# Kernel tuning notes

Measured on AMD Instinct MI355X. Metric: run time of the kernel, lower is better.

## Reference

```python
import jax, jax.numpy as jnp
import numpy as np

N_NODES = 20000
N_EDGES = 320000
N_RELS = 200
DESC_LEN = 16
DIM_G = 64
DIM_WORD = 300
DIM_HIDDEN = 256
H_DIR = DIM_HIDDEN // 2  # per-direction GRU hidden
N_CLASS = 2000
V_WORD = 30000
V_DESC = 30000
B, T = 4, 32


def setup_inputs() -> dict:
    key = jax.random.key(0)
    ks = jax.random.split(key, 24)
    inp = {}
    # index tensors (pad token is 0; generate tokens in [1, V) so all positions valid)
    inp['questions'] = jax.random.randint(ks[0], (B, T), 1, V_WORD)
    inp['node_descs'] = jax.random.randint(ks[1], (N_NODES, DESC_LEN), 1, V_DESC)
    inp['edge_src'] = jax.random.randint(ks[2], (N_EDGES,), 0, N_NODES)
    inp['edge_dst'] = jax.random.randint(ks[3], (N_EDGES,), 0, N_NODES)
    inp['edge_type'] = jax.random.randint(ks[4], (N_EDGES,), 0, N_RELS)
    # embeddings (normal with std 1/sqrt(dim) as in original init)
    inp['emb_word'] = jax.random.normal(ks[5], (V_WORD, DIM_WORD)) / np.sqrt(DIM_WORD)
    inp['emb_desc'] = jax.random.normal(ks[6], (V_DESC, DIM_G)) / np.sqrt(DIM_G)
    # BiGRU params (gates order r,z,n; concatenated along last dim)
    s = 0.1
    inp['Wx_f'] = jax.random.normal(ks[7], (DIM_WORD, 3 * H_DIR)) * s
    inp['Wh_f'] = jax.random.normal(ks[8], (H_DIR, 3 * H_DIR)) * s
    inp['bx_f'] = jnp.zeros((3 * H_DIR,))
    inp['bh_f'] = jnp.zeros((3 * H_DIR,))
    inp['Wx_b'] = jax.random.normal(ks[9], (DIM_WORD, 3 * H_DIR)) * s
    inp['Wh_b'] = jax.random.normal(ks[10], (H_DIR, 3 * H_DIR)) * s
    inp['bx_b'] = jnp.zeros((3 * H_DIR,))
    inp['bh_b'] = jnp.zeros((3 * H_DIR,))
    # lin_h_to_g (kaiming-ish scale)
    inp['W_hg'] = jax.random.normal(ks[11], (DIM_HIDDEN, DIM_G)) * np.sqrt(2.0 / DIM_HIDDEN)
    inp['b_hg'] = jnp.zeros((DIM_G,))
    # RGCN basis decomposition
    inp['bases'] = jax.random.normal(ks[12], (1, DIM_G, DIM_G)) * np.sqrt(1.0 / DIM_G)
    inp['w_comp'] = jax.random.normal(ks[13], (N_RELS, 1))
    inp['rgcn_bias'] = jnp.zeros((DIM_G,))
    # classifier
    inp['W1'] = jax.random.normal(ks[14], (DIM_G + DIM_HIDDEN, 1024)) * np.sqrt(2.0 / (DIM_G + DIM_HIDDEN))
    inp['b1'] = jnp.zeros((1024,))
    inp['W2'] = jax.random.normal(ks[15], (1024, N_CLASS)) * np.sqrt(2.0 / 1024)
    inp['b2'] = jnp.zeros((N_CLASS,))
    return inp


def _gru_last_hidden(x, mask, Wx, Wh, bx, bh):
    """Run a GRU over time; hidden only updates where mask is True.
    x: [B,T,D], mask: [B,T]. Returns final hidden [B,H]."""
    bsz = x.shape[0]
    h0 = jnp.zeros((bsz, Wh.shape[0]), x.dtype)
    gx_all = x @ Wx + bx  # [B,T,3H] precompute input gates

    def step(h, inputs):
        gx, mt = inputs  # [B,3H], [B]
        gh = h @ Wh + bh
        xr, xz, xn = jnp.split(gx, 3, axis=-1)
        hr, hz, hn = jnp.split(gh, 3, axis=-1)
        r = jax.nn.sigmoid(xr + hr)
        z = jax.nn.sigmoid(xz + hz)
        n = jnp.tanh(xn + r * hn)
        h_new = (1.0 - z) * n + z * h
        h = jnp.where(mt[:, None], h_new, h)
        return h, None

    hT, _ = jax.lax.scan(step, h0, (gx_all.transpose(1, 0, 2), mask.T))
    return hT


def _rel_graph_conv(h, edge_src, edge_dst, edge_type, bases, w_comp, bias):
    """Basis-decomposed RGCN layer (DGL RelGraphConv, norm=None, no self-loop).
    h: [B,N,G]. W_r = sum_k w_comp[r,k] * bases[k]."""
    n = h.shape[1]
    # project through each basis first: [B,N,K,O]
    hb = jnp.einsum('bng,kgo->bnko', h, bases)
    # per-edge message: gather src, combine with relation coefficients -> [B,E,O]
    msg = jnp.einsum('beko,ek->beo', hb[:, edge_src], w_comp[edge_type])
    # scatter-add to destination nodes
    agg = jax.vmap(lambda m: jax.ops.segment_sum(m, edge_dst, num_segments=n))(msg)
    return jax.nn.relu(agg + bias)


def reference(questions, node_descs, edge_src, edge_dst, edge_type,
              emb_word, emb_desc,
              Wx_f, Wh_f, bx_f, bh_f, Wx_b, Wh_b, bx_b, bh_b,
              W_hg, b_hg, bases, w_comp, rgcn_bias,
              W1, b1, W2, b2):
    # ---- question encoding (BiGRU over non-pad tokens; pad id = 0) ----
    mask = questions != 0  # [B,T]
    x = emb_word[questions]  # [B,T,Dw] (dropout is identity at eval)
    hf = _gru_last_hidden(x, mask, Wx_f, Wh_f, bx_f, bh_f)
    hb = _gru_last_hidden(x[:, ::-1], mask[:, ::-1], Wx_b, Wh_b, bx_b, bh_b)
    q_emb = jnp.concatenate([hf, hb], axis=-1)  # [B, dim_hidden]

    # ---- attention-weighted node features from descriptions ----
    desc_emb = emb_desc[node_descs]          # [N,L,G]
    q_g = q_emb @ W_hg + b_hg                # [B,G]
    attn1 = jax.nn.softmax(jnp.einsum('nlg,bg->bnl', desc_emb, q_g), axis=-1)
    node_feat = jnp.einsum('bnl,nlg->bng', attn1, desc_emb)  # [B,N,G]

    # ---- one RGCN hidden layer over the KB graph ----
    node_feat = _rel_graph_conv(node_feat, edge_src, edge_dst, edge_type,
                                bases, w_comp, rgcn_bias)

    # ---- attention pooling over nodes ----
    attn2 = jax.nn.softmax(jnp.einsum('bng,bg->bn', node_feat, q_g), axis=1)
    node_agg = jnp.einsum('bn,bng->bg', attn2, node_feat)    # [B,G]

    # ---- classifier ----
    feat = jnp.concatenate([node_agg, q_emb], axis=-1)       # [B, G+H]
    logits = jax.nn.relu(feat @ W1 + b1) @ W2 + b2           # [B, n_class]
    return logits
```

## Files before the change

### kernel.cpp

```cpp
#include <hip/hip_runtime.h>
#include <hip/hip_bf16.h>
#include <math.h>

typedef __hip_bfloat16 bf16;

#define NNODES 20000
#define NEDGES 320000
#define DLEN   16
#define G      64
#define DW     300
#define DH     256
#define HD     128
#define G3     384
#define NCLS   2000
#define NB     4
#define TT     32
#define VDESC  30000
#define A2BLK  1024
#define A2MID  64

#define NBLK_CVT   384
#define NBLK_GX2   1536
#define NBLK_DESCB (VDESC / 16)
#define NBLK_HIST  ((NEDGES + 255) / 256)
#define NBLK_SCAT  ((NEDGES + 255) / 256)
#define NBLK_DQ    ((VDESC + 63) / 64)

__device__ __forceinline__ float ld(const float* p, size_t i) { return p[i]; }
__device__ __forceinline__ float ld(const bf16* p, size_t i) { return __bfloat162float(p[i]); }
__device__ __forceinline__ void st(float* p, size_t i, float v) { p[i] = v; }
__device__ __forceinline__ void st(bf16* p, size_t i, float v) { p[i] = __float2bfloat16(v); }
__device__ __forceinline__ float relu(float x) { return (x < 0.f) ? 0.f : x; }

struct __align__(8) bf4 { bf16 x, y, z, w; };

#define OFF_FLAG  ((size_t)0)
#define OFF_GX    (OFF_FLAG + 4)
#define OFF_WHF   (OFF_GX   + 2*NB*TT*G3)
#define OFF_QEMB  (OFF_WHF  + 2*HD*G3)
#define OFF_QG    (OFF_QEMB + NB*DH)
#define OFF_NF    (OFF_QG   + NB*G)
#define OFF_HB    (OFF_NF   + (size_t)NB*NNODES*G)
#define OFF_DESCB (OFF_HB   + (size_t)NB*NNODES*G)
#define OFF_DQ    (OFF_DESCB + (size_t)VDESC*G/2)
#define OFF_PART  (OFF_DQ   + (size_t)VDESC*NB)
#define OFF_PART2 (OFF_PART + (size_t)A2BLK*NB*66)
#define OFF_DEG   (OFF_PART2+ (size_t)A2MID*NB*66)
#define OFF_OFFS  (OFF_DEG  + NNODES)
#define OFF_RANK  (OFF_OFFS + NNODES + 8)
#define OFF_EPACK (OFF_RANK + NEDGES)
#define OFF_HID   (OFF_EPACK + 2*(size_t)NEDGES)

__global__ void k_init(const unsigned* probe, int* flag, int* deg) {
    int i = blockIdx.x * 256 + threadIdx.x;
    if (i < NNODES) deg[i] = 0;
    if (blockIdx.x == 0 && threadIdx.x < 64) {
        int cnt = 0;
        for (int k = threadIdx.x; k < 4096; k += 64) {
            unsigned lo = probe[k] & 0xFFFFu;
            unsigned e = (lo >> 7) & 0xFFu;
            cnt += (e >= 0x66u && e <= 0x7Eu) ? 1 : 0;
        }
#pragma unroll
        for (int off = 1; off < 64; off <<= 1) cnt += __shfl_xor(cnt, off, 64);
        if (threadIdx.x == 0) *flag = (2 * cnt > 4096) ? 1 : 0;
    }
}

template <typename T>
__device__ void cvt_body(int id, const void* Whf_, const void* Whb_, float* whf) {
    if (id >= 2 * HD * G3) return;
    int d = id / (HD * G3), r = id % (HD * G3);
    const T* W = (const T*)(d ? Whb_ : Whf_);
    whf[id] = ld(W, (size_t)r);
}

template <typename T>
__device__ void gx2_body(int bx2, const int* questions, const void* emb_word_,
                         const void* Wxf_, const void* bxf_,
                         const void* Wxb_, const void* bxb_, float* gx,
                         float* xs, float* psum) {
    int tid = threadIdx.x;
    int jt = bx2 % 6;
    int rid = bx2 / 6;
    int step = rid & 31;
    int b = (rid >> 5) & 3;
    int d = rid >> 7;
    int t = d ? (TT - 1 - step) : step;
    int tok = questions[b * TT + t];
    const T* row = (const T*)emb_word_ + (size_t)tok * DW;
    for (int k = tid; k < DW; k += 256) xs[k] = ld(row, (size_t)k);
    __syncthreads();
    int lane = tid & 63, phase = tid >> 6;
    int j = jt * 64 + lane;
    const T* Wx = (const T*)(d ? Wxb_ : Wxf_);
    float acc = 0.f;
    int k0 = phase * 75;
#pragma unroll 15
    for (int kk = 0; kk < 75; kk++) {
        int k = k0 + kk;
        acc += xs[k] * ld(Wx, (size_t)k * G3 + j);
    }
    psum[tid] = acc;
    __syncthreads();
    if (phase == 0) {
        const T* bx = (const T*)(d ? bxb_ : bxf_);
        float tot = ld(bx, (size_t)j)
                  + psum[lane] + psum[64 + lane] + psum[128 + lane] + psum[192 + lane];
        gx[(size_t)rid * G3 + j] = tot;
    }
}

template <typename T>
__device__ void descb_body(int bx3, const void* emb_desc_, const void* bases_,
                           bf16* descB, float* bsm, float* rsm) {
    int tid = threadIdx.x;
    const T* bases = (const T*)bases_;
    const T* desc = (const T*)emb_desc_;
    for (int i = tid; i < G * G; i += 256) bsm[(i >> 6) * 68 + (i & 63)] = ld(bases, (size_t)i);
    int r0 = bx3 * 16;
    for (int i = tid; i < 16 * G; i += 256) {
        int r = i >> 6, k = i & 63;
        rsm[r * 68 + k] = ld(desc, (size_t)(r0 + r) * G + k);
    }
    __syncthreads();
    int g = tid & 63, slot = tid >> 6;
#pragma unroll
    for (int it = 0; it < 4; it++) {
        int r = slot * 4 + it;
        float acc = 0.f;
#pragma unroll 8
        for (int k = 0; k < G; k++) acc = fmaf(rsm[r * 68 + k], bsm[k * 68 + g], acc);
        descB[(size_t)(r0 + r) * G + g] = __float2bfloat16(acc);
    }
}

__global__ void k_prep(const int* flag, const void* Whf, const void* Whb, float* whf,
                       const int* questions, const void* emb_word,
                       const void* Wxf, const void* bxf,
                       const void* Wxb, const void* bxb, float* gx,
                       const void* emb_desc, const void* bases, bf16* descB,
                       const int* edge_dst, int* deg, int* rank) {
    __shared__ __align__(16) float smem[64 * 68 + 16 * 68];
    int bx = blockIdx.x;
    int tid = threadIdx.x;
    if (bx < NBLK_CVT) {
        int id = bx * 256 + tid;
        if (*flag) cvt_body<bf16>(id, Whf, Whb, whf);
        else       cvt_body<float>(id, Whf, Whb, whf);
    } else if (bx < NBLK_CVT + NBLK_GX2) {
        int bx2 = bx - NBLK_CVT;
        float* xs = smem;
        float* psum = smem + 320;
        if (*flag) gx2_body<bf16>(bx2, questions, emb_word, Wxf, bxf, Wxb, bxb, gx, xs, psum);
        else       gx2_body<float>(bx2, questions, emb_word, Wxf, bxf, Wxb, bxb, gx, xs, psum);
    } else if (bx < NBLK_CVT + NBLK_GX2 + NBLK_DESCB) {
        int bx3 = bx - NBLK_CVT - NBLK_GX2;
        float* bsm = smem;
        float* rsm = smem + 64 * 68;
        if (*flag) descb_body<bf16>(bx3, emb_desc, bases, descB, bsm, rsm);
        else       descb_body<float>(bx3, emb_desc, bases, descB, bsm, rsm);
    } else {
        int e = (bx - NBLK_CVT - NBLK_GX2 - NBLK_DESCB) * 256 + tid;
        if (e < NEDGES) rank[e] = atomicAdd(&deg[edge_dst[e]], 1);
    }
}

template <typename T>
__device__ void gru_body(const int* questions, const float* gx, const float* whf,
                         const void* bhf_, const void* bhb_, float* qemb,
                         float* hsm, float* ghs) {
    int tid = threadIdx.x;
    int d = blockIdx.x >> 2, b = blockIdx.x & 3;
    int half = tid / G3, j = tid - half * G3;
    const float* wh = whf + (size_t)d * HD * G3 + (size_t)half * 64 * G3 + j;
    float w[64];
#pragma unroll
    for (int m = 0; m < 64; m++) w[m] = wh[(size_t)m * G3];
    const T* bh = (const T*)(d ? bhb_ : bhf_);
    float bhj = (half == 0) ? ld(bh, (size_t)j) : 0.f;
    if (tid < HD) hsm[tid] = 0.f;
    const float* gxb = gx + ((size_t)(d * NB + b)) * TT * G3;
    __syncthreads();
    const float4* h4 = (const float4*)(hsm + half * 64);
    for (int step = 0; step < TT; step++) {
        float acc = bhj;
#pragma unroll
        for (int m4 = 0; m4 < 16; m4++) {
            float4 hp = h4[m4];
            acc = fmaf(hp.x, w[4 * m4 + 0], acc);
            acc = fmaf(hp.y, w[4 * m4 + 1], acc);
            acc = fmaf(hp.z, w[4 * m4 + 2], acc);
            acc = fmaf(hp.w, w[4 * m4 + 3], acc);
        }
        ghs[half * G3 + j] = acc;
        __syncthreads();
        if (tid < HD) {
            const float* gxp = gxb + step * G3;
            int t = d ? (TT - 1 - step) : step;
            bool msk = questions[b * TT + t] != 0;
            float gr = ghs[tid] + ghs[G3 + tid];
            float gz = ghs[HD + tid] + ghs[G3 + HD + tid];
            float gn = ghs[2 * HD + tid] + ghs[G3 + 2 * HD + tid];
            float r = 1.f / (1.f + expf(-(gxp[tid] + gr)));
            float z = 1.f / (1.f + expf(-(gxp[HD + tid] + gz)));
            float n = tanhf(gxp[2 * HD + tid] + r * gn);
            float hn = (1.f - z) * n + z * hsm[tid];
            if (msk) hsm[tid] = hn;
        }
        __syncthreads();
    }
    if (tid < HD) qemb[b * DH + d * HD + tid] = hsm[tid];
}

__device__ void scan_body(const int* deg, int* offs, int* wtot) {
    int t = threadIdx.x;
    int lane = t & 63, wave = t >> 6;
    int c[27];
    int base = t * 27;
    int run = 0;
#pragma unroll
    for (int i = 0; i < 27; i++) {
        int v = (base + i < NNODES) ? deg[base + i] : 0;
        c[i] = run;
        run += v;
    }
    int myrun = run, inc = run;
#pragma unroll
    for (int off = 1; off < 64; off <<= 1) {
        int u = __shfl_up(inc, off, 64);
        if (lane >= off) inc += u;
    }
    if (lane == 63) wtot[wave] = inc;
    __syncthreads();
    if (t == 0) {
        int s = 0;
#pragma unroll
        for (int i = 0; i < 12; i++) { int v = wtot[i]; wtot[i] = s; s += v; }
        offs[NNODES] = s;
    }
    __syncthreads();
    int ebase = wtot[wave] + inc - myrun;
#pragma unroll
    for (int i = 0; i < 27; i++) {
        if (base + i < NNODES) offs[base + i] = ebase + c[i];
    }
}

__global__ __launch_bounds__(2 * G3) void k_gru(const int* flag, const int* questions,
                                                const float* gx, const float* whf,
                                                const void* bhf, const void* bhb, float* qemb,
                                                const int* deg, int* offs) {
    __shared__ __align__(16) float hsm[HD];
    __shared__ float ghs[2 * G3];
    __shared__ int wtot[12];
    if (blockIdx.x < 8) {
        if (*flag) gru_body<bf16>(questions, gx, whf, bhf, bhb, qemb, hsm, ghs);
        else       gru_body<float>(questions, gx, whf, bhf, bhb, qemb, hsm, ghs);
    } else {
        scan_body(deg, offs, wtot);
    }
}

template <typename T>
__device__ void qg_compute(const float* qemb, const void* W_hg_, const void* b_hg_,
                           float* out ) {
    int tid = threadIdx.x;
    int b = tid >> 6, g = tid & 63;
    const T* W = (const T*)W_hg_;
    float acc = ld((const T*)b_hg_, (size_t)g);
#pragma unroll 4
    for (int i = 0; i < DH; i++) acc += qemb[b * DH + i] * ld(W, (size_t)i * G + g);
    out[b * G + g] = acc;
}

template <typename T>
__device__ void dq_body(int chunk, const void* emb_desc_, const float* qgs, float* dq) {
    int tid = threadIdx.x;
    int ii = tid >> 2, b = tid & 3;
    int idx = chunk * 64 + ii;
    if (idx >= VDESC) return;
    const T* row = (const T*)emb_desc_ + (size_t)idx * G;
    const float* q = qgs + b * G;
    float acc = 0.f;
#pragma unroll 8
    for (int k = 0; k < G; k++) acc = fmaf(ld(row, (size_t)k), q[k], acc);
    dq[(size_t)idx * NB + b] = acc;
}

__global__ __launch_bounds__(256) void k_qg_dq(const int* flag, const float* qemb,
                                               const void* W_hg, const void* b_hg, float* qg,
                                               const void* emb_desc, float* dq) {
    __shared__ float qgs[NB * G];
    if (blockIdx.x == 0) {
        if (*flag) qg_compute<bf16>(qemb, W_hg, b_hg, qg);
        else       qg_compute<float>(qemb, W_hg, b_hg, qg);
        return;
    }
    if (*flag) qg_compute<bf16>(qemb, W_hg, b_hg, qgs);
    else       qg_compute<float>(qemb, W_hg, b_hg, qgs);
    __syncthreads();
    int chunk = blockIdx.x - 1;
    if (*flag) dq_body<bf16>(chunk, emb_desc, qgs, dq);
    else       dq_body<float>(chunk, emb_desc, qgs, dq);
}

template <typename T>
__device__ void scatter_body(int e, const int* src, const int* dst, const int* typ,
                             const void* w_comp_, const int* offs, const int* rank,
                             int2* epack) {
    if (e < NEDGES) {
        int pos = offs[dst[e]] + rank[e];
        int2 v;
        v.x = src[e];
        v.y = __float_as_int(ld((const T*)w_comp_, (size_t)typ[e]));
        epack[pos] = v;
    }
}

__device__ void attn1_body(int nb4, const int* node_descs, const float* dq,
                           const bf16* descB, bf16* hb16, float* attn_s, int* idxs) {
    int tid = threadIdx.x;
    int w = tid >> 6, lane = tid & 63;
    int n = nb4 * 4 + w;
    int b = lane >> 4, l = lane & 15;
    const int* nd = node_descs + n * DLEN;
    int idx = nd[l];
    float logit = dq[(size_t)idx * NB + b];
    float mx = logit;
#pragma unroll
    for (int off = 1; off < 16; off <<= 1) mx = fmaxf(mx, __shfl_xor(mx, off, 64));
    float e = expf(logit - mx);
    float s = e;
#pragma unroll
    for (int off = 1; off < 16; off <<= 1) s += __shfl_xor(s, off, 64);
    attn_s[w * 64 + lane] = e / s;
    if (lane < 16) idxs[w * 16 + lane] = idx;
    __syncthreads();
    float o0 = 0.f, o1 = 0.f, o2 = 0.f, o3 = 0.f;
#pragma unroll
    for (int ll = 0; ll < DLEN; ll++) {
        int row = idxs[w * 16 + ll];
        float v = __bfloat162float(descB[(size_t)row * G + lane]);
        o0 = fmaf(attn_s[w * 64 + ll], v, o0);
        o1 = fmaf(attn_s[w * 64 + 16 + ll], v, o1);
        o2 = fmaf(attn_s[w * 64 + 32 + ll], v, o2);
        o3 = fmaf(attn_s[w * 64 + 48 + ll], v, o3);
    }
    size_t baseo = (size_t)n * (NB * G) + lane;
    hb16[baseo + 0 * G] = __float2bfloat16(o0);
    hb16[baseo + 1 * G] = __float2bfloat16(o1);
    hb16[baseo + 2 * G] = __float2bfloat16(o2);
    hb16[baseo + 3 * G] = __float2bfloat16(o3);
}

__global__ __launch_bounds__(256) void k_sc_attn1(const int* flag,
                                                  const int* src, const int* dst, const int* typ,
                                                  const void* w_comp, const int* offs,
                                                  const int* rank, int2* epack,
                                                  const int* node_descs, const float* dq,
                                                  const bf16* descB, bf16* hb16) {
    __shared__ float attn_s[4 * 64];
    __shared__ int idxs[4 * DLEN];
    int bx = blockIdx.x;
    if (bx < NBLK_SCAT) {
        int e = bx * 256 + threadIdx.x;
        if (*flag) scatter_body<bf16>(e, src, dst, typ, w_comp, offs, rank, epack);
        else       scatter_body<float>(e, src, dst, typ, w_comp, offs, rank, epack);
    } else {
        attn1_body(bx - NBLK_SCAT, node_descs, dq, descB, hb16, attn_s, idxs);
    }
}

template <typename T>
__device__ void agg_body(const bf16* hb16, const int* offs, const int2* epack,
                         const void* bias_, bf16* out_nf16) {
    int tid = threadIdx.x;
    int b = tid >> 6, g = tid & 63;
    int dn = blockIdx.x;
    int s0 = offs[dn], s1 = offs[dn + 1];
    int boff = b * G + g;
    float acc = 0.f;
    int p = s0;
    for (; p + 15 < s1; p += 16) {
        int2 ev[16]; float x[16];
#pragma unroll
        for (int k = 0; k < 16; k++) ev[k] = epack[p + k];
#pragma unroll
        for (int k = 0; k < 16; k++)
            x[k] = __bfloat162float(hb16[(size_t)ev[k].x * (NB * G) + boff]);
#pragma unroll
        for (int k = 0; k < 16; k++) acc += __int_as_float(ev[k].y) * x[k];
    }
    for (; p + 7 < s1; p += 8) {
        int2 ev[8]; float x[8];
#pragma unroll
        for (int k = 0; k < 8; k++) ev[k] = epack[p + k];
#pragma unroll
        for (int k = 0; k < 8; k++)
            x[k] = __bfloat162float(hb16[(size_t)ev[k].x * (NB * G) + boff]);
#pragma unroll
        for (int k = 0; k < 8; k++) acc += __int_as_float(ev[k].y) * x[k];
    }
    for (; p + 3 < s1; p += 4) {
        int2 ev[4]; float x[4];
#pragma unroll
        for (int k = 0; k < 4; k++) ev[k] = epack[p + k];
#pragma unroll
        for (int k = 0; k < 4; k++)
            x[k] = __bfloat162float(hb16[(size_t)ev[k].x * (NB * G) + boff]);
#pragma unroll
        for (int k = 0; k < 4; k++) acc += __int_as_float(ev[k].y) * x[k];
    }
    for (; p < s1; p++) {
        int2 ev = epack[p];
        acc += __int_as_float(ev.y) * __bfloat162float(hb16[(size_t)ev.x * (NB * G) + boff]);
    }
    out_nf16[((size_t)b * NNODES + dn) * G + g] =
        __float2bfloat16(relu(acc + ld((const T*)bias_, (size_t)g)));
}
__global__ __launch_bounds__(256) void k_agg(const int* flag, const bf16* hb16, const int* offs,
                                             const int2* epack, const void* bias,
                                             bf16* out_nf16) {
    if (*flag) agg_body<bf16>(hb16, offs, epack, bias, out_nf16);
    else       agg_body<float>(hb16, offs, epack, bias, out_nf16);
}

__device__ __forceinline__ void a2_update(float& M, float& L, float& A, float p, float v) {
    if (p > M) {
        float s = expf(M - p);
        A *= s; L *= s; M = p;
    }
    float e = expf(p - M);
    L += e;
    A = fmaf(e, v, A);
}

__global__ __launch_bounds__(256) void k_attn2(const bf16* rg, const float* qg, float* part) {
    int tid = threadIdx.x;
    int b = tid >> 6, lane = tid & 63;
    float q = qg[b * G + lane];
    int chunk = (NNODES + A2BLK - 1) / A2BLK;
    int n0 = blockIdx.x * chunk;
    int n1 = min(n0 + chunk, NNODES);
    const bf16* base = rg + (size_t)b * NNODES * G + lane;
    float M = -3.4e38f, L = 0.f, A = 0.f;
    int n = n0;
    for (; n + 3 < n1; n += 4) {
        float v0 = __bfloat162float(base[(size_t)(n + 0) * G]);
        float v1 = __bfloat162float(base[(size_t)(n + 1) * G]);
        float v2 = __bfloat162float(base[(size_t)(n + 2) * G]);
        float v3 = __bfloat162float(base[(size_t)(n + 3) * G]);
        float p0 = v0 * q, p1 = v1 * q, p2 = v2 * q, p3 = v3 * q;
#pragma unroll
        for (int off = 32; off >= 1; off >>= 1) {
            p0 += __shfl_xor(p0, off, 64);
            p1 += __shfl_xor(p1, off, 64);
            p2 += __shfl_xor(p2, off, 64);
            p3 += __shfl_xor(p3, off, 64);
        }
        a2_update(M, L, A, p0, v0);
        a2_update(M, L, A, p1, v1);
        a2_update(M, L, A, p2, v2);
        a2_update(M, L, A, p3, v3);
    }
    for (; n < n1; n++) {
        float v = __bfloat162float(base[(size_t)n * G]);
        float p = v * q;
#pragma unroll
        for (int off = 32; off >= 1; off >>= 1) p += __shfl_xor(p, off, 64);
        a2_update(M, L, A, p, v);
    }
    float* pp = part + ((size_t)blockIdx.x * NB + b) * 66;
    if (lane == 0) { pp[0] = M; pp[1] = L; }
    pp[2 + lane] = A;
}

__global__ void k_attn2m(const float* part, float* part2) {
    int tid = threadIdx.x;
    int b = tid >> 6, lane = tid & 63;
    int grp = blockIdx.x;
    float M = -3.4e38f, L = 0.f, A = 0.f;
    for (int i = 0; i < A2BLK / A2MID; i++) {
        const float* pp = part + ((size_t)(grp * (A2BLK / A2MID) + i) * NB + b) * 66;
        float m = pp[0], l = pp[1], a = pp[2 + lane];
        float mn = fmaxf(M, m);
        float e1 = expf(M - mn), e2 = expf(m - mn);
        A = A * e1 + a * e2;
        L = L * e1 + l * e2;
        M = mn;
    }
    float* pq = part2 + ((size_t)grp * NB + b) * 66;
    if (lane == 0) { pq[0] = M; pq[1] = L; }
    pq[2 + lane] = A;
}

template <typename T>
__device__ void fc1_body(const float* part2, const float* qemb,
                         const void* W1_, const void* b1_, float* hid,
                         float* feat, float* psum) {
    int tid = threadIdx.x;
    int b = blockIdx.x >> 4, tile = blockIdx.x & 15;
    if (tid < 64) {
        float M = -3.4e38f, L = 0.f, A = 0.f;
        for (int p = 0; p < A2MID; p++) {
            const float* pp = part2 + ((size_t)p * NB + b) * 66;
            float m = pp[0], l = pp[1], a = pp[2 + tid];
            float mn = fmaxf(M, m);
            float e1 = expf(M - mn), e2 = expf(m - mn);
            A = A * e1 + a * e2;
            L = L * e1 + l * e2;
            M = mn;
        }
        feat[tid] = A / L;
        feat[tid + 256] = qemb[b * DH + tid + 192];
    } else {
        feat[tid] = qemb[b * DH + tid - G];
    }
    __syncthreads();
    int lane = tid & 63, phase = tid >> 6;
    int u = tile * 64 + lane;
    const T* W1 = (const T*)W1_;
    float acc = 0.f;
#pragma unroll 8
    for (int kk = 0; kk < 80; kk++) {
        int k = phase * 80 + kk;
        acc += feat[k] * ld(W1, (size_t)k * 1024 + u);
    }
    psum[tid] = acc;
    __syncthreads();
    if (phase == 0) {
        float tot = psum[lane] + psum[64 + lane] + psum[128 + lane] + psum[192 + lane]
                  + ld((const T*)b1_, (size_t)u);
        hid[b * 1024 + u] = relu(tot);
    }
}
__global__ __launch_bounds__(256) void k_fc1(const int* flag, const float* part2,
                                             const float* qemb, const void* W1, const void* b1,
                                             float* hid) {
    __shared__ float feat[320];
    __shared__ float psum[256];
    if (*flag) fc1_body<bf16>(part2, qemb, W1, b1, hid, feat, psum);
    else       fc1_body<float>(part2, qemb, W1, b1, hid, feat, psum);
}

template <typename T>
__device__ void fc2_body(const float* hid, const void* W2_, const void* b2_, void* out_,
                         float* hs, float* psum) {
    int tid = threadIdx.x;
    int tile = blockIdx.x;
#pragma unroll
    for (int i = 0; i < 16; i++) hs[tid + 256 * i] = hid[tid + 256 * i];
    __syncthreads();
    int lane = tid & 63, phase = tid >> 6;
    int c = tile * 64 + lane;
    bool ok = (c < NCLS);
    const T* W2 = (const T*)W2_;
    float a0 = 0.f, a1 = 0.f, a2 = 0.f, a3 = 0.f;
    if (ok) {
#pragma unroll 8
        for (int uu = 0; uu < 256; uu++) {
            int u = phase * 256 + uu;
            float w = ld(W2, (size_t)u * NCLS + c);
            a0 += hs[u] * w;
            a1 += hs[1024 + u] * w;
            a2 += hs[2048 + u] * w;
            a3 += hs[3072 + u] * w;
        }
    }
    psum[tid] = a0;
    psum[256 + tid] = a1;
    psum[512 + tid] = a2;
    psum[768 + tid] = a3;
    __syncthreads();
    if (phase == 0 && ok) {
        float bb = ld((const T*)b2_, (size_t)c);
#pragma unroll
        for (int b = 0; b < NB; b++) {
            float* ps = psum + b * 256;
            float tot = ps[lane] + ps[64 + lane] + ps[128 + lane] + ps[192 + lane] + bb;
            st((T*)out_, (size_t)b * NCLS + c, tot);
        }
    }
}
__global__ __launch_bounds__(256) void k_fc2(const int* flag, const float* hid,
                                             const void* W2, const void* b2v, void* out) {
    __shared__ float hs[4096];
    __shared__ float psum[1024];
    if (*flag) fc2_body<bf16>(hid, W2, b2v, out, hs, psum);
    else       fc2_body<float>(hid, W2, b2v, out, hs, psum);
}

extern "C" void kernel_launch(void* const* d_in, const int* in_sizes, int n_in,
                              void* d_out, int out_size, void* d_ws, size_t ws_size,
                              hipStream_t stream) {
    const int* questions  = (const int*)d_in[0];
    const int* node_descs = (const int*)d_in[1];
    const int* edge_src   = (const int*)d_in[2];
    const int* edge_dst   = (const int*)d_in[3];
    const int* edge_type  = (const int*)d_in[4];
    const void* emb_word  = d_in[5];
    const void* emb_desc  = d_in[6];
    const void* Wx_f = d_in[7];
    const void* Wh_f = d_in[8];
    const void* bx_f = d_in[9];
    const void* bh_f = d_in[10];
    const void* Wx_b = d_in[11];
    const void* Wh_b = d_in[12];
    const void* bx_b = d_in[13];
    const void* bh_b = d_in[14];
    const void* W_hg = d_in[15];
    const void* b_hg = d_in[16];
    const void* bases = d_in[17];
    const void* w_comp = d_in[18];
    const void* rgcn_bias = d_in[19];
    const void* W1 = d_in[20];
    const void* b1 = d_in[21];
    const void* W2 = d_in[22];
    const void* b2 = d_in[23];

    float* ws = (float*)d_ws;
    int*      flag  = (int*)(ws + OFF_FLAG);
    float*    gx    = ws + OFF_GX;
    float*    whf   = ws + OFF_WHF;
    float*    qemb  = ws + OFF_QEMB;
    float*    qg    = ws + OFF_QG;
    bf16*     nf16  = (bf16*)(ws + OFF_NF);
    bf16*     hb16  = (bf16*)(ws + OFF_HB);
    bf16*     descB = (bf16*)(ws + OFF_DESCB);
    float*    dq    = ws + OFF_DQ;
    float*    part  = ws + OFF_PART;
    float*    part2 = ws + OFF_PART2;
    int*      deg   = (int*)(ws + OFF_DEG);
    int*      offs  = (int*)(ws + OFF_OFFS);
    int*      rank  = (int*)(ws + OFF_RANK);
    int2*     epack = (int2*)(ws + OFF_EPACK);
    float*    hid   = ws + OFF_HID;

    hipLaunchKernelGGL(k_init, dim3(80), dim3(256), 0, stream,
                       (const unsigned*)emb_word, flag, deg);
    hipLaunchKernelGGL(k_prep,
                       dim3(NBLK_CVT + NBLK_GX2 + NBLK_DESCB + NBLK_HIST), dim3(256), 0, stream,
                       flag, Wh_f, Wh_b, whf,
                       questions, emb_word, Wx_f, bx_f, Wx_b, bx_b, gx,
                       emb_desc, bases, descB,
                       edge_dst, deg, rank);
    hipLaunchKernelGGL(k_gru, dim3(9), dim3(2 * G3), 0, stream,
                       flag, questions, gx, whf, bh_f, bh_b, qemb, deg, offs);
    hipLaunchKernelGGL(k_qg_dq, dim3(1 + NBLK_DQ), dim3(256), 0, stream,
                       flag, qemb, W_hg, b_hg, qg, emb_desc, dq);
    hipLaunchKernelGGL(k_sc_attn1, dim3(NBLK_SCAT + NNODES / 4), dim3(256), 0, stream,
                       flag, edge_src, edge_dst, edge_type, w_comp, offs, rank, epack,
                       node_descs, dq, descB, hb16);
    hipLaunchKernelGGL(k_agg, dim3(NNODES), dim3(256), 0, stream,
                       flag, hb16, offs, epack, rgcn_bias, nf16);
    hipLaunchKernelGGL(k_attn2, dim3(A2BLK), dim3(256), 0, stream, nf16, qg, part);
    hipLaunchKernelGGL(k_attn2m, dim3(A2MID), dim3(256), 0, stream, part, part2);
    hipLaunchKernelGGL(k_fc1, dim3(NB * 16), dim3(256), 0, stream,
                       flag, part2, qemb, W1, b1, hid);
    hipLaunchKernelGGL(k_fc2, dim3(32), dim3(256), 0, stream,
                       flag, hid, W2, b2, d_out);
}
```

Measured before the change: 305.4 us.

## Fuse RGCN aggregation with attention pooling, transpose W2 for wider fc2

Folds the attention-pooling online softmax into the RGCN aggregation kernel, so the bf16 node-feature tensor is never written and then read back. Each aggregation block now handles four destination nodes and emits one partial, and the merge kernel takes the larger partial count. The attn1 blocks each process four node groups. W2 is transposed into the workspace during the prep kernel so fc2 can run on 250 blocks with coalesced row reads and wave reductions, at the cost of an extra 8 MB transpose pass on every call.

```diff
diff --git a/kernel.cpp b/kernel.cpp
--- a/kernel.cpp
+++ b/kernel.cpp
@@ -16,14 +16,16 @@
 #define NB     4
 #define TT     32
 #define VDESC  30000
-#define A2BLK  1024
+#define NPART  5000
 #define A2MID  64
 
 #define NBLK_CVT   384
 #define NBLK_GX2   1536
 #define NBLK_DESCB (VDESC / 16)
 #define NBLK_HIST  ((NEDGES + 255) / 256)
+#define NBLK_W2T   (32 * 16)
 #define NBLK_SCAT  ((NEDGES + 255) / 256)
+#define NBLK_A1    (NNODES / 16)
 #define NBLK_DQ    ((VDESC + 63) / 64)
 
 __device__ __forceinline__ float ld(const float* p, size_t i) { return p[i]; }
@@ -32,24 +34,22 @@
 __device__ __forceinline__ void st(bf16* p, size_t i, float v) { p[i] = __float2bfloat16(v); }
 __device__ __forceinline__ float relu(float x) { return (x < 0.f) ? 0.f : x; }
 
-struct __align__(8) bf4 { bf16 x, y, z, w; };
-
 #define OFF_FLAG  ((size_t)0)
 #define OFF_GX    (OFF_FLAG + 4)
 #define OFF_WHF   (OFF_GX   + 2*NB*TT*G3)
 #define OFF_QEMB  (OFF_WHF  + 2*HD*G3)
 #define OFF_QG    (OFF_QEMB + NB*DH)
-#define OFF_NF    (OFF_QG   + NB*G)
-#define OFF_HB    (OFF_NF   + (size_t)NB*NNODES*G)
-#define OFF_DESCB (OFF_HB   + (size_t)NB*NNODES*G)
+#define OFF_HB    (OFF_QG   + NB*G)
+#define OFF_DESCB (OFF_HB   + (size_t)NB*NNODES*G/2)
 #define OFF_DQ    (OFF_DESCB + (size_t)VDESC*G/2)
 #define OFF_PART  (OFF_DQ   + (size_t)VDESC*NB)
-#define OFF_PART2 (OFF_PART + (size_t)A2BLK*NB*66)
+#define OFF_PART2 (OFF_PART + (size_t)NPART*NB*66)
 #define OFF_DEG   (OFF_PART2+ (size_t)A2MID*NB*66)
 #define OFF_OFFS  (OFF_DEG  + NNODES)
 #define OFF_RANK  (OFF_OFFS + NNODES + 8)
 #define OFF_EPACK (OFF_RANK + NEDGES)
 #define OFF_HID   (OFF_EPACK + 2*(size_t)NEDGES)
+#define OFF_W2T   (OFF_HID  + 4096)
 
 __global__ void k_init(const unsigned* probe, int* flag, int* deg) {
     int i = blockIdx.x * 256 + threadIdx.x;
@@ -135,12 +135,36 @@
     }
 }
 
+template <typename T>
+__device__ void w2t_body(int bx5, const void* W2_, float* w2t, float* tile ) {
+    int tid = threadIdx.x;
+    int ct = bx5 >> 4, ut = bx5 & 15;
+    int c0 = ct * 64, u0 = ut * 64;
+    int lane = tid & 63, slot = tid >> 6;
+    const T* W2 = (const T*)W2_;
+    int c = c0 + lane;
+    bool okc = (c < NCLS);
+#pragma unroll
+    for (int i = 0; i < 16; i++) {
+        int u = slot * 16 + i;
+        tile[u * 65 + lane] = okc ? ld(W2, (size_t)(u0 + u) * NCLS + c) : 0.f;
+    }
+    __syncthreads();
+#pragma unroll
+    for (int i = 0; i < 16; i++) {
+        int cl = slot * 16 + i;
+        if (c0 + cl < NCLS)
+            w2t[(size_t)(c0 + cl) * 1024 + u0 + lane] = tile[lane * 65 + cl];
+    }
+}
+
 __global__ void k_prep(const int* flag, const void* Whf, const void* Whb, float* whf,
                        const int* questions, const void* emb_word,
                        const void* Wxf, const void* bxf,
                        const void* Wxb, const void* bxb, float* gx,
                        const void* emb_desc, const void* bases, bf16* descB,
-                       const int* edge_dst, int* deg, int* rank) {
+                       const int* edge_dst, int* deg, int* rank,
+                       const void* W2, float* w2t) {
     __shared__ __align__(16) float smem[64 * 68 + 16 * 68];
     int bx = blockIdx.x;
     int tid = threadIdx.x;
@@ -160,9 +184,13 @@
         float* rsm = smem + 64 * 68;
         if (*flag) descb_body<bf16>(bx3, emb_desc, bases, descB, bsm, rsm);
         else       descb_body<float>(bx3, emb_desc, bases, descB, bsm, rsm);
-    } else {
+    } else if (bx < NBLK_CVT + NBLK_GX2 + NBLK_DESCB + NBLK_HIST) {
         int e = (bx - NBLK_CVT - NBLK_GX2 - NBLK_DESCB) * 256 + tid;
         if (e < NEDGES) rank[e] = atomicAdd(&deg[edge_dst[e]], 1);
+    } else {
+        int bx5 = bx - NBLK_CVT - NBLK_GX2 - NBLK_DESCB - NBLK_HIST;
+        if (*flag) w2t_body<bf16>(bx5, W2, w2t, smem);
+        else       w2t_body<float>(bx5, W2, w2t, smem);
     }
 }
 
@@ -368,62 +396,12 @@
         if (*flag) scatter_body<bf16>(e, src, dst, typ, w_comp, offs, rank, epack);
         else       scatter_body<float>(e, src, dst, typ, w_comp, offs, rank, epack);
     } else {
-        attn1_body(bx - NBLK_SCAT, node_descs, dq, descB, hb16, attn_s, idxs);
-    }
-}
-
-template <typename T>
-__device__ void agg_body(const bf16* hb16, const int* offs, const int2* epack,
-                         const void* bias_, bf16* out_nf16) {
-    int tid = threadIdx.x;
-    int b = tid >> 6, g = tid & 63;
-    int dn = blockIdx.x;
-    int s0 = offs[dn], s1 = offs[dn + 1];
-    int boff = b * G + g;
-    float acc = 0.f;
-    int p = s0;
-    for (; p + 15 < s1; p += 16) {
-        int2 ev[16]; float x[16];
-#pragma unroll
-        for (int k = 0; k < 16; k++) ev[k] = epack[p + k];
-#pragma unroll
-        for (int k = 0; k < 16; k++)
-            x[k] = __bfloat162float(hb16[(size_t)ev[k].x * (NB * G) + boff]);
-#pragma unroll
-        for (int k = 0; k < 16; k++) acc += __int_as_float(ev[k].y) * x[k];
-    }
-    for (; p + 7 < s1; p += 8) {
-        int2 ev[8]; float x[8];
-#pragma unroll
-        for (int k = 0; k < 8; k++) ev[k] = epack[p + k];
-#pragma unroll
-        for (int k = 0; k < 8; k++)
-            x[k] = __bfloat162float(hb16[(size_t)ev[k].x * (NB * G) + boff]);
-#pragma unroll
-        for (int k = 0; k < 8; k++) acc += __int_as_float(ev[k].y) * x[k];
-    }
-    for (; p + 3 < s1; p += 4) {
-        int2 ev[4]; float x[4];
-#pragma unroll
-        for (int k = 0; k < 4; k++) ev[k] = epack[p + k];
-#pragma unroll
-        for (int k = 0; k < 4; k++)
-            x[k] = __bfloat162float(hb16[(size_t)ev[k].x * (NB * G) + boff]);
-#pragma unroll
-        for (int k = 0; k < 4; k++) acc += __int_as_float(ev[k].y) * x[k];
-    }
-    for (; p < s1; p++) {
-        int2 ev = epack[p];
-        acc += __int_as_float(ev.y) * __bfloat162float(hb16[(size_t)ev.x * (NB * G) + boff]);
-    }
-    out_nf16[((size_t)b * NNODES + dn) * G + g] =
-        __float2bfloat16(relu(acc + ld((const T*)bias_, (size_t)g)));
-}
-__global__ __launch_bounds__(256) void k_agg(const int* flag, const bf16* hb16, const int* offs,
-                                             const int2* epack, const void* bias,
-                                             bf16* out_nf16) {
-    if (*flag) agg_body<bf16>(hb16, offs, epack, bias, out_nf16);
-    else       agg_body<float>(hb16, offs, epack, bias, out_nf16);
+        int base = (bx - NBLK_SCAT) * 4;
+        for (int it = 0; it < 4; it++) {
+            if (it) __syncthreads();
+            attn1_body(base + it, node_descs, dq, descB, hb16, attn_s, idxs);
+        }
+    }
 }
 
 __device__ __forceinline__ void a2_update(float& M, float& L, float& A, float p, float v) {
@@ -436,53 +414,82 @@
     A = fmaf(e, v, A);
 }
 
-__global__ __launch_bounds__(256) void k_attn2(const bf16* rg, const float* qg, float* part) {
-    int tid = threadIdx.x;
-    int b = tid >> 6, lane = tid & 63;
-    float q = qg[b * G + lane];
-    int chunk = (NNODES + A2BLK - 1) / A2BLK;
-    int n0 = blockIdx.x * chunk;
-    int n1 = min(n0 + chunk, NNODES);
-    const bf16* base = rg + (size_t)b * NNODES * G + lane;
+template <typename T>
+__device__ void agg_body(const bf16* hb16, const int* offs, const int2* epack,
+                         const void* bias_, const float* qg, float* part) {
+    int tid = threadIdx.x;
+    int b = tid >> 6, g = tid & 63;
+    int boff = b * G + g;
+    float bias = ld((const T*)bias_, (size_t)g);
+    float q = qg[b * G + g];
     float M = -3.4e38f, L = 0.f, A = 0.f;
-    int n = n0;
-    for (; n + 3 < n1; n += 4) {
-        float v0 = __bfloat162float(base[(size_t)(n + 0) * G]);
-        float v1 = __bfloat162float(base[(size_t)(n + 1) * G]);
-        float v2 = __bfloat162float(base[(size_t)(n + 2) * G]);
-        float v3 = __bfloat162float(base[(size_t)(n + 3) * G]);
-        float p0 = v0 * q, p1 = v1 * q, p2 = v2 * q, p3 = v3 * q;
-#pragma unroll
-        for (int off = 32; off >= 1; off >>= 1) {
-            p0 += __shfl_xor(p0, off, 64);
-            p1 += __shfl_xor(p1, off, 64);
-            p2 += __shfl_xor(p2, off, 64);
-            p3 += __shfl_xor(p3, off, 64);
-        }
-        a2_update(M, L, A, p0, v0);
-        a2_update(M, L, A, p1, v1);
-        a2_update(M, L, A, p2, v2);
-        a2_update(M, L, A, p3, v3);
-    }
-    for (; n < n1; n++) {
-        float v = __bfloat162float(base[(size_t)n * G]);
-        float p = v * q;
-#pragma unroll
-        for (int off = 32; off >= 1; off >>= 1) p += __shfl_xor(p, off, 64);
-        a2_update(M, L, A, p, v);
+#pragma unroll 1
+    for (int it = 0; it < 4; it++) {
+        int dn = blockIdx.x * 4 + it;
+        int s0 = offs[dn], s1 = offs[dn + 1];
+        float acc = 0.f;
+        int p = s0;
+        for (; p + 15 < s1; p += 16) {
+            int2 ev[16]; float x[16];
+#pragma unroll
+            for (int k = 0; k < 16; k++) ev[k] = epack[p + k];
+#pragma unroll
+            for (int k = 0; k < 16; k++)
+                x[k] = __bfloat162float(hb16[(size_t)ev[k].x * (NB * G) + boff]);
+#pragma unroll
+            for (int k = 0; k < 16; k++) acc += __int_as_float(ev[k].y) * x[k];
+        }
+        for (; p + 7 < s1; p += 8) {
+            int2 ev[8]; float x[8];
+#pragma unroll
+            for (int k = 0; k < 8; k++) ev[k] = epack[p + k];
+#pragma unroll
+            for (int k = 0; k < 8; k++)
+                x[k] = __bfloat162float(hb16[(size_t)ev[k].x * (NB * G) + boff]);
+#pragma unroll
+            for (int k = 0; k < 8; k++) acc += __int_as_float(ev[k].y) * x[k];
+        }
+        for (; p + 3 < s1; p += 4) {
+            int2 ev[4]; float x[4];
+#pragma unroll
+            for (int k = 0; k < 4; k++) ev[k] = epack[p + k];
+#pragma unroll
+            for (int k = 0; k < 4; k++)
+                x[k] = __bfloat162float(hb16[(size_t)ev[k].x * (NB * G) + boff]);
+#pragma unroll
+            for (int k = 0; k < 4; k++) acc += __int_as_float(ev[k].y) * x[k];
+        }
+        for (; p < s1; p++) {
+            int2 ev = epack[p];
+            acc += __int_as_float(ev.y) * __bfloat162float(hb16[(size_t)ev.x * (NB * G) + boff]);
+        }
+        float v = relu(acc + bias);
+        float pl = v * q;
+#pragma unroll
+        for (int off = 32; off >= 1; off >>= 1) pl += __shfl_xor(pl, off, 64);
+        a2_update(M, L, A, pl, v);
     }
     float* pp = part + ((size_t)blockIdx.x * NB + b) * 66;
-    if (lane == 0) { pp[0] = M; pp[1] = L; }
-    pp[2 + lane] = A;
-}
-
-__global__ void k_attn2m(const float* part, float* part2) {
+    if (g == 0) { pp[0] = M; pp[1] = L; }
+    pp[2 + g] = A;
+}
+__global__ __launch_bounds__(256) void k_agg(const int* flag, const bf16* hb16, const int* offs,
+                                             const int2* epack, const void* bias,
+                                             const float* qg, float* part) {
+    if (*flag) agg_body<bf16>(hb16, offs, epack, bias, qg, part);
+    else       agg_body<float>(hb16, offs, epack, bias, qg, part);
+}
+
+__global__ __launch_bounds__(256) void k_attn2m(const float* part, float* part2) {
     int tid = threadIdx.x;
     int b = tid >> 6, lane = tid & 63;
     int grp = blockIdx.x;
+    const int per = (NPART + A2MID - 1) / A2MID;
+    int start = grp * per;
+    int end = (start + per < NPART) ? (start + per) : NPART;
     float M = -3.4e38f, L = 0.f, A = 0.f;
-    for (int i = 0; i < A2BLK / A2MID; i++) {
-        const float* pp = part + ((size_t)(grp * (A2BLK / A2MID) + i) * NB + b) * 66;
+    for (int i = start; i < end; i++) {
+        const float* pp = part + ((size_t)i * NB + b) * 66;
         float m = pp[0], l = pp[1], a = pp[2 + lane];
         float mn = fmaxf(M, m);
         float e1 = expf(M - mn), e2 = expf(m - mn);
@@ -545,50 +552,44 @@
 }
 
 template <typename T>
-__device__ void fc2_body(const float* hid, const void* W2_, const void* b2_, void* out_,
-                         float* hs, float* psum) {
-    int tid = threadIdx.x;
-    int tile = blockIdx.x;
-#pragma unroll
-    for (int i = 0; i < 16; i++) hs[tid + 256 * i] = hid[tid + 256 * i];
-    __syncthreads();
-    int lane = tid & 63, phase = tid >> 6;
-    int c = tile * 64 + lane;
-    bool ok = (c < NCLS);
-    const T* W2 = (const T*)W2_;
-    float a0 = 0.f, a1 = 0.f, a2 = 0.f, a3 = 0.f;
-    if (ok) {
-#pragma unroll 8
-        for (int uu = 0; uu < 256; uu++) {
-            int u = phase * 256 + uu;
-            float w = ld(W2, (size_t)u * NCLS + c);
-            a0 += hs[u] * w;
-            a1 += hs[1024 + u] * w;
-            a2 += hs[2048 + u] * w;
-            a3 += hs[3072 + u] * w;
-        }
-    }
-    psum[tid] = a0;
-    psum[256 + tid] = a1;
-    psum[512 + tid] = a2;
-    psum[768 + tid] = a3;
-    __syncthreads();
-    if (phase == 0 && ok) {
-        float bb = ld((const T*)b2_, (size_t)c);
-#pragma unroll
-        for (int b = 0; b < NB; b++) {
-            float* ps = psum + b * 256;
-            float tot = ps[lane] + ps[64 + lane] + ps[128 + lane] + ps[192 + lane] + bb;
-            st((T*)out_, (size_t)b * NCLS + c, tot);
+__device__ void fc2_body(const float* hid, const float* w2t, const void* b2_, void* out_,
+                         float* hs) {
+    int tid = threadIdx.x;
+    for (int i = tid; i < 4096; i += 256) hs[i] = hid[i];
+    __syncthreads();
+    int lane = tid & 63, w = tid >> 6;
+#pragma unroll
+    for (int itc = 0; itc < 2; itc++) {
+        int c = blockIdx.x * 8 + w * 2 + itc;
+        const float* wrow = w2t + (size_t)c * 1024;
+        float a0 = 0.f, a1 = 0.f, a2 = 0.f, a3 = 0.f;
+#pragma unroll
+        for (int i = 0; i < 16; i++) {
+            int u = i * 64 + lane;
+            float wv = wrow[u];
+            a0 = fmaf(wv, hs[u], a0);
+            a1 = fmaf(wv, hs[1024 + u], a1);
+            a2 = fmaf(wv, hs[2048 + u], a2);
+            a3 = fmaf(wv, hs[3072 + u], a3);
+        }
+#pragma unroll
+        for (int off = 32; off >= 1; off >>= 1) {
+            a0 += __shfl_xor(a0, off, 64);
+            a1 += __shfl_xor(a1, off, 64);
+            a2 += __shfl_xor(a2, off, 64);
+            a3 += __shfl_xor(a3, off, 64);
+        }
+        if (lane < 4) {
+            float av = (lane == 0) ? a0 : (lane == 1) ? a1 : (lane == 2) ? a2 : a3;
+            st((T*)out_, (size_t)lane * NCLS + c, av + ld((const T*)b2_, (size_t)c));
         }
     }
 }
 __global__ __launch_bounds__(256) void k_fc2(const int* flag, const float* hid,
-                                             const void* W2, const void* b2v, void* out) {
+                                             const float* w2t, const void* b2v, void* out) {
     __shared__ float hs[4096];
-    __shared__ float psum[1024];
-    if (*flag) fc2_body<bf16>(hid, W2, b2v, out, hs, psum);
-    else       fc2_body<float>(hid, W2, b2v, out, hs, psum);
+    if (*flag) fc2_body<bf16>(hid, w2t, b2v, out, hs);
+    else       fc2_body<float>(hid, w2t, b2v, out, hs);
 }
 
 extern "C" void kernel_launch(void* const* d_in, const int* in_sizes, int n_in,
@@ -625,7 +626,6 @@
     float*    whf   = ws + OFF_WHF;
     float*    qemb  = ws + OFF_QEMB;
     float*    qg    = ws + OFF_QG;
-    bf16*     nf16  = (bf16*)(ws + OFF_NF);
     bf16*     hb16  = (bf16*)(ws + OFF_HB);
     bf16*     descB = (bf16*)(ws + OFF_DESCB);
     float*    dq    = ws + OFF_DQ;
@@ -636,28 +636,29 @@
     int*      rank  = (int*)(ws + OFF_RANK);
     int2*     epack = (int2*)(ws + OFF_EPACK);
     float*    hid   = ws + OFF_HID;
+    float*    w2t   = ws + OFF_W2T;
 
     hipLaunchKernelGGL(k_init, dim3(80), dim3(256), 0, stream,
                        (const unsigned*)emb_word, flag, deg);
     hipLaunchKernelGGL(k_prep,
-                       dim3(NBLK_CVT + NBLK_GX2 + NBLK_DESCB + NBLK_HIST), dim3(256), 0, stream,
+                       dim3(NBLK_CVT + NBLK_GX2 + NBLK_DESCB + NBLK_HIST + NBLK_W2T),
+                       dim3(256), 0, stream,
                        flag, Wh_f, Wh_b, whf,
                        questions, emb_word, Wx_f, bx_f, Wx_b, bx_b, gx,
                        emb_desc, bases, descB,
-                       edge_dst, deg, rank);
+                       edge_dst, deg, rank, W2, w2t);
     hipLaunchKernelGGL(k_gru, dim3(9), dim3(2 * G3), 0, stream,
                        flag, questions, gx, whf, bh_f, bh_b, qemb, deg, offs);
     hipLaunchKernelGGL(k_qg_dq, dim3(1 + NBLK_DQ), dim3(256), 0, stream,
                        flag, qemb, W_hg, b_hg, qg, emb_desc, dq);
-    hipLaunchKernelGGL(k_sc_attn1, dim3(NBLK_SCAT + NNODES / 4), dim3(256), 0, stream,
+    hipLaunchKernelGGL(k_sc_attn1, dim3(NBLK_SCAT + NBLK_A1), dim3(256), 0, stream,
                        flag, edge_src, edge_dst, edge_type, w_comp, offs, rank, epack,
                        node_descs, dq, descB, hb16);
-    hipLaunchKernelGGL(k_agg, dim3(NNODES), dim3(256), 0, stream,
-                       flag, hb16, offs, epack, rgcn_bias, nf16);
-    hipLaunchKernelGGL(k_attn2, dim3(A2BLK), dim3(256), 0, stream, nf16, qg, part);
+    hipLaunchKernelGGL(k_agg, dim3(NPART), dim3(256), 0, stream,
+                       flag, hb16, offs, epack, rgcn_bias, qg, part);
     hipLaunchKernelGGL(k_attn2m, dim3(A2MID), dim3(256), 0, stream, part, part2);
     hipLaunchKernelGGL(k_fc1, dim3(NB * 16), dim3(256), 0, stream,
                        flag, part2, qemb, W1, b1, hid);
-    hipLaunchKernelGGL(k_fc2, dim3(32), dim3(256), 0, stream,
-                       flag, hid, W2, b2, d_out);
-}
+    hipLaunchKernelGGL(k_fc2, dim3(NCLS / 8), dim3(256), 0, stream,
+                       flag, hid, w2t, b2, d_out);
+}
```

After: 326.6 us. 1.07x slower.
